# Kernel tuning notes

Measured on AMD Instinct MI355X. Metric: run time of the kernel, lower is better.

Reference implementation:

```python
import jax, jax.numpy as jnp
import numpy as np
from jax import lax

E = 16          # num_experts
CAP = 256       # capacity
MAX_IT = 3      # max_iterations
LPF = 2.0       # load_penalty_factor
DTEMP = 2.0     # diversity_temp
MIN_USAGE = 0.05
NC = 10         # num_classes
TC = 256        # trunk_channels
B = 2048
MIN_TOK = max(1, int(B * MIN_USAGE))        # 102
K_STATIC = min(B, max(CAP, MIN_TOK))        # static top-k width per expert claim


def setup_inputs() -> dict:
    key = jax.random.key(0)
    ks = jax.random.split(key, 16)
    d = {}
    d['x'] = jax.random.normal(ks[0], (B, 3, 32, 32), jnp.float32)
    chans = [(3, 32), (32, 64), (64, 128), (128, 256)]
    for i, (ci, co) in enumerate(chans, 1):
        d[f'cw{i}'] = jax.random.normal(ks[i], (co, ci, 3, 3), jnp.float32) * (1.0 / np.sqrt(ci * 9))
        d[f'cb{i}'] = jnp.zeros((co,), jnp.float32)
        d[f'g{i}'] = jnp.ones((co,), jnp.float32)
        d[f'be{i}'] = jnp.zeros((co,), jnp.float32)
        d[f'm{i}'] = jnp.zeros((co,), jnp.float32)
        d[f'v{i}'] = jnp.ones((co,), jnp.float32)
    d['gw1'] = jax.random.normal(ks[5], (E, TC, TC // 2), jnp.float32) * 0.05
    d['gb1'] = jnp.zeros((E, TC // 2), jnp.float32)
    d['gw2'] = jax.random.normal(ks[6], (E, TC // 2), jnp.float32) * 0.05
    d['gb2'] = jnp.zeros((E,), jnp.float32)
    d['cls_w'] = jax.random.normal(ks[7], (E, NC, TC), jnp.float32) * 0.01
    d['cls_b'] = jnp.zeros((E, NC), jnp.float32)
    d['usage_ema'] = jnp.ones((E,), jnp.float32) / E
    return d


def _conv_bn_relu(x, w, b, g, beta, m, v):
    y = lax.conv_general_dilated(x, w, (1, 1), 'SAME', dimension_numbers=('NCHW', 'OIHW', 'NCHW'))
    y = y + b[None, :, None, None]
    scale = (g / jnp.sqrt(v + 1e-5))[None, :, None, None]
    return jax.nn.relu((y - m[None, :, None, None]) * scale + beta[None, :, None, None])


def _maxpool2(x):
    return lax.reduce_window(x, -jnp.inf, lax.max, (1, 1, 2, 2), (1, 1, 2, 2), 'VALID')


def _forward(x, cw1, cb1, g1, be1, m1, v1, cw2, cb2, g2, be2, m2, v2,
             cw3, cb3, g3, be3, m3, v3, cw4, cb4, g4, be4, m4, v4,
             gw1, gb1, gw2, gb2, cls_w, cls_b, usage_ema):
    # trunk (eval-mode BN)
    h = _conv_bn_relu(x, cw1, cb1, g1, be1, m1, v1)
    h = _conv_bn_relu(h, cw2, cb2, g2, be2, m2, v2)
    h = _maxpool2(h)
    h = _conv_bn_relu(h, cw3, cb3, g3, be3, m3, v3)
    h = _conv_bn_relu(h, cw4, cb4, g4, be4, m4, v4)
    h = _maxpool2(h)
    feats = h.mean(axis=(2, 3))  # AdaptiveAvgPool2d(1)+Flatten -> [B, TC]

    # per-expert classifier heads
    logits_e = jnp.einsum('bd,ecd->bec', feats, cls_w) + cls_b[None]  # [B,E,NC]
    probs = jax.nn.softmax(logits_e, axis=2)
    ent = -(probs * jnp.log(jnp.clip(probs, 1e-12))).sum(axis=2)      # [B,E]
    confidence = -ent

    # per-expert gates (vectorized over experts); dropout is identity in eval
    hidden = jax.nn.relu(jnp.einsum('bd,edh->beh', feats, gw1) + gb1[None])
    expert_scores = (jnp.einsum('beh,eh->be', hidden, gw2) + gb2[None]) / DTEMP

    routing_scores = 0.6 * expert_scores + 0.4 * confidence - LPF * usage_ema[None]

    # iterative capacity-constrained routing (eval: expert order 0..E-1)
    D = jnp.zeros((B, E), bool)
    loads = jnp.zeros((E,), jnp.float32)
    avail = jnp.ones((B,), bool)
    ranks = jnp.arange(K_STATIC)
    for it in range(MAX_IT):
        # penalty from loads at the START of the iteration
        pscores = routing_scores - (it + 1) * LPF * loads[None]
        for j in range(E):
            sj = jnp.where(avail, pscores[:, j], -jnp.inf)
            vc = avail.sum().astype(jnp.int32)
            rc = jnp.maximum(0, CAP - loads[j].astype(jnp.int32))
            ntc = jnp.where((rc == 0) | (vc == 0), 0,
                            jnp.maximum(jnp.minimum(rc, vc), jnp.minimum(MIN_TOK, vc)))
            _, idx = lax.top_k(sj, K_STATIC)
            take = ranks < ntc
            claimed = jnp.zeros((B,), bool).at[idx].set(take)
            D = D.at[:, j].set(D[:, j] | claimed)
            avail = avail & ~claimed
            loads = loads.at[j].add(ntc.astype(jnp.float32))

    # fallback: sequentially assign leftover tokens to least-loaded of top-3
    def fb(carry, inp):
        Dc, lc = carry
        sc, av, i = inp
        _, t3 = lax.top_k(sc, 3)
        best = t3[jnp.argmin(lc[t3])]
        Dc = Dc.at[i, best].set(Dc[i, best] | av)
        lc = lc.at[best].add(av.astype(jnp.float32))
        return (Dc, lc), None

    (D, loads), _ = lax.scan(fb, (D, loads), (routing_scores, avail, jnp.arange(B)))

    Df = D.astype(jnp.float32)
    active = routing_scores * Df
    active = active - active.max(axis=1, keepdims=True)
    weights = jax.nn.softmax(active + (Df - 1.0) * 1e9, axis=1)
    final_logits = (weights[:, :, None] * logits_e).sum(axis=1)
    return final_logits, routing_scores, D


def reference(x, cw1, cb1, g1, be1, m1, v1, cw2, cb2, g2, be2, m2, v2,
              cw3, cb3, g3, be3, m3, v3, cw4, cb4, g4, be4, m4, v4,
              gw1, gb1, gw2, gb2, cls_w, cls_b, usage_ema):
    return _forward(x, cw1, cb1, g1, be1, m1, v1, cw2, cb2, g2, be2, m2, v2,
                    cw3, cb3, g3, be3, m3, v3, cw4, cb4, g4, be4, m4, v4,
                    gw1, gb1, gw2, gb2, cls_w, cls_b, usage_ema)
```

## Files before the change

kernel.cpp:

```cpp
#include <hip/hip_runtime.h>

typedef __attribute__((ext_vector_type(8))) short short8;
typedef __attribute__((ext_vector_type(4))) float f32x4;

__device__ __forceinline__ unsigned short f2bf(float f) {
  unsigned u = __float_as_uint(f);
  unsigned r = (u + 0x7fffu + ((u >> 16) & 1u)) >> 16;
  return (unsigned short)r;
}
__device__ __forceinline__ float bf2f(unsigned short h) {
  return __uint_as_float(((unsigned)h) << 16);
}

__global__ __launch_bounds__(256) void bnprep_kernel(
    const float* __restrict__ g, const float* __restrict__ be,
    const float* __restrict__ m, const float* __restrict__ v,
    const float* __restrict__ b, float* __restrict__ A, float* __restrict__ C, int n)
{
  int i = blockIdx.x * 256 + threadIdx.x;
  if (i < n) {
    float s = g[i] / sqrtf(v[i] + 1e-5f);
    A[i] = s;
    C[i] = (b[i] - m[i]) * s + be[i];
  }
}

__global__ __launch_bounds__(256) void wprep2_kernel(
    const float* __restrict__ w, unsigned short* __restrict__ wPk, int CO, int CI)
{
  int NCB = CI / 32, NF = CO / 16;
  int total = 9 * NCB * NF * 64;
  int idx = blockIdx.x * 256 + threadIdx.x;
  if (idx >= total) return;
  int lane = idx & 63;
  int unit = idx >> 6;
  int f = unit % NF;
  int cb = (unit / NF) % NCB;
  int s = unit / (NF * NCB);
  int co = f * 16 + (lane & 15);
  int ci0 = cb * 32 + (lane >> 4) * 8;
  long base = (long)unit * 1024 + lane * 8;
  #pragma unroll
  for (int j = 0; j < 8; ++j) {
    float v = w[((long)co * CI + ci0 + j) * 9 + s];
    unsigned short h = f2bf(v);
    unsigned short l = f2bf(v - bf2f(h));
    wPk[base + j] = h;
    wPk[base + 512 + j] = l;
  }
}

__global__ __launch_bounds__(512, 2) void conv12_kernel(
    const float* __restrict__ xin, const float* __restrict__ cw1,
    const float* __restrict__ A1p, const float* __restrict__ C1p,
    const unsigned short* __restrict__ wPk, const float* __restrict__ Ap,
    const float* __restrict__ Cp, unsigned short* __restrict__ outA)
{
  constexpr int TY = 16, TX = 32;
  constexpr int PXW = TX + 2;
  constexpr int PXT = (TY + 2) * PXW;
  constexpr int PLSTR = PXT * 8 + 8;
  constexpr int NF = 4;
  __shared__ alignas(16) unsigned short smem[8 * PLSTR];
  __shared__ alignas(16) float sx[2160];
  __shared__ alignas(16) float sw[864];

  const int nwg = gridDim.x;
  const int orig = blockIdx.x;
  const int q = nwg >> 3, r = nwg & 7;
  const int xcd = orig & 7, pos = orig >> 3;
  const int bx = (xcd < r ? xcd * (q + 1) : r * (q + 1) + (xcd - r) * q) + pos;

  const int img = bx >> 1;
  const int tY0 = (bx & 1) * 16;

  const int tid = threadIdx.x;
  const int lane = tid & 63;
  const int lx = lane & 15, kg = lane >> 4;
  const int w = tid >> 6;

  for (int i = tid; i < 2160; i += 512) {
    int c = i / 720, rem = i - c * 720;
    int yy = rem / 36, xx2 = rem - yy * 36;
    int gy = tY0 + yy - 2, gx = xx2 - 2;
    sx[i] = (gy >= 0 && gy < 32 && gx >= 0 && gx < 32)
            ? xin[(long)img * 3072 + c * 1024 + gy * 32 + gx] : 0.f;
  }
  for (int i = tid; i < 864; i += 512) {
    int co = i & 31, kk = i >> 5;
    sw[kk * 32 + co] = cw1[(long)co * 27 + kk];
  }
  __syncthreads();

  #pragma unroll 1
  for (int p = 0; p < 2; ++p) {
    int px = p * 512 + tid;
    if (px < PXT) {
      int ry = px / PXW, rx = px - ry * PXW;
      int gy = tY0 + ry - 1, gx = rx - 1;
      if (gy >= 0 && gy < 32 && gx >= 0 && gx < 32) {
        #pragma unroll 1
        for (int half = 0; half < 2; ++half) {
          float acc[16];
          #pragma unroll
          for (int j = 0; j < 16; ++j) acc[j] = 0.f;
          #pragma unroll
          for (int c = 0; c < 3; ++c) {
            #pragma unroll
            for (int k = 0; k < 9; ++k) {
              int dy = k / 3, dx = k - 3 * (k / 3);
              float iv = sx[c * 720 + (ry + dy) * 36 + rx + dx];
              const float4* w4 = (const float4*)(sw + (c * 9 + k) * 32 + half * 16);
              #pragma unroll
              for (int q2 = 0; q2 < 4; ++q2) {
                float4 wv = w4[q2];
                acc[4 * q2 + 0] += iv * wv.x; acc[4 * q2 + 1] += iv * wv.y;
                acc[4 * q2 + 2] += iv * wv.z; acc[4 * q2 + 3] += iv * wv.w;
              }
            }
          }
          #pragma unroll
          for (int j2 = 0; j2 < 2; ++j2) {
            short8 hv, lv;
            #pragma unroll
            for (int j = 0; j < 8; ++j) {
              int co = half * 16 + j2 * 8 + j;
              float vv = fmaxf(acc[j2 * 8 + j] * A1p[co] + C1p[co], 0.f);
              unsigned short h = f2bf(vv);
              hv[j] = (short)h;
              lv[j] = (short)f2bf(vv - bf2f(h));
            }
            int plane = half * 2 + j2;
            *(short8*)(smem + plane * PLSTR + px * 8) = hv;
            *(short8*)(smem + (plane + 4) * PLSTR + px * 8) = lv;
          }
        }
      } else {
        short8 zz = {0, 0, 0, 0, 0, 0, 0, 0};
        #pragma unroll
        for (int cc = 0; cc < 8; ++cc)
          *(short8*)(smem + cc * PLSTR + px * 8) = zz;
      }
    }
  }
  __syncthreads();

  f32x4 acc[4][4];
  #pragma unroll
  for (int i = 0; i < 4; ++i)
    #pragma unroll
    for (int j = 0; j < 4; ++j) acc[i][j] = (f32x4){0.f, 0.f, 0.f, 0.f};

  for (int s = 0; s < 9; ++s) {
    const int ky = s / 3, kx = s - 3 * (s / 3);
    const long ub = ((long)(s * NF)) * 1024 + lane * 8;
    short8 bh[4], bl[4];
    #pragma unroll
    for (int nf = 0; nf < 4; ++nf) {
      bh[nf] = *(const short8*)(wPk + ub + nf * 1024);
      bl[nf] = *(const short8*)(wPk + ub + nf * 1024 + 512);
    }
    #pragma unroll
    for (int mf = 0; mf < 4; ++mf) {
      const int yoff = mf >> 1;
      const int xb = (mf & 1) * 16;
      const int y = w * 2 + yoff;
      const int pxa = (y + ky) * PXW + xb + kx + lx;
      short8 ah = *(const short8*)(smem + kg * PLSTR + pxa * 8);
      short8 al = *(const short8*)(smem + (kg + 4) * PLSTR + pxa * 8);
      #pragma unroll
      for (int nf = 0; nf < 4; ++nf)
        acc[mf][nf] = __builtin_amdgcn_mfma_f32_16x16x32_bf16(ah, bh[nf], acc[mf][nf], 0, 0, 0);
      #pragma unroll
      for (int nf = 0; nf < 4; ++nf)
        acc[mf][nf] = __builtin_amdgcn_mfma_f32_16x16x32_bf16(ah, bl[nf], acc[mf][nf], 0, 0, 0);
      #pragma unroll
      for (int nf = 0; nf < 4; ++nf)
        acc[mf][nf] = __builtin_amdgcn_mfma_f32_16x16x32_bf16(al, bh[nf], acc[mf][nf], 0, 0, 0);
    }
  }
  __syncthreads();

  float Ar[4], Cr[4];
  #pragma unroll
  for (int nf = 0; nf < 4; ++nf) {
    int co = nf * 16 + lx;
    Ar[nf] = Ap[co]; Cr[nf] = Cp[co];
  }

  unsigned short* slice = smem + w * 2048;
  const int py = (tY0 >> 1) + w;
  #pragma unroll
  for (int xf = 0; xf < 2; ++xf) {
    #pragma unroll
    for (int rp = 0; rp < 2; ++rp) {
      int ox = xf * 8 + 2 * kg + rp;
      #pragma unroll
      for (int nf = 0; nf < 4; ++nf) {
        float v0 = fmaxf(fmaxf(acc[xf][nf][2 * rp], acc[xf][nf][2 * rp + 1]),
                         fmaxf(acc[xf + 2][nf][2 * rp], acc[xf + 2][nf][2 * rp + 1]));
        float vv = fmaxf(v0 * Ar[nf] + Cr[nf], 0.f);
        unsigned short h = f2bf(vv);
        unsigned short l = f2bf(vv - bf2f(h));
        slice[(ox * 2 + 0) * 64 + nf * 16 + lx] = h;
        slice[(ox * 2 + 1) * 64 + nf * 16 + lx] = l;
      }
    }
  }
  #pragma unroll
  for (int v = 0; v < 4; ++v) {
    int hoff = lane * 8 + v * 512;
    int x2 = hoff >> 7, rem = hoff & 127;
    int seg = rem >> 6, inner = rem & 63;
    short8 d = *(const short8*)(slice + hoff);
    *(short8*)(outA + ((long)img * 256 + py * 16 + x2) * 128 + seg * 64 + inner) = d;
  }
}

template<int H, int CI, int CO, int COB, int TY, int TX, int MODE>
__global__ __launch_bounds__(512, 2) void convmf4_kernel(
    const unsigned short* __restrict__ actIn, const unsigned short* __restrict__ wPk,
    const float* __restrict__ Ap, const float* __restrict__ Cp,
    void* __restrict__ outP)
{
  constexpr int NCB = CI / 32;
  constexpr int NF  = CO / 16;
  constexpr int NCOG = COB / 64;
  constexpr int NPXG = 8 / NCOG;
  constexpr int ROWS_PG = TY / NPXG;
  constexpr int FRX = TX / 16;
  constexpr int PXW = TX + 2;
  constexpr int PXT = (TY + 2) * PXW;
  constexpr int PLSTR = PXT * 8 + 8;
  constexpr int TILES_Y = H / TY;
  constexpr int CBLK = CO / COB;
  constexpr int TPI = TILES_Y * CBLK;
  constexpr int PIX_IN = 2 * CI;
  __shared__ alignas(16) unsigned short smem[8 * PLSTR];

  const int nwg = gridDim.x;
  const int orig = blockIdx.x;
  const int q = nwg >> 3, r = nwg & 7;
  const int xcd = orig & 7, pos = orig >> 3;
  const int bx = (xcd < r ? xcd * (q + 1) : r * (q + 1) + (xcd - r) * q) + pos;

  const int img = bx / TPI;
  const int sub = bx % TPI;
  const int tY0 = (sub % TILES_Y) * TY;
  const int blkco = sub / TILES_Y;

  const int tid = threadIdx.x;
  const int lane = tid & 63;
  const int lx = lane & 15, kg = lane >> 4;
  const int w = tid >> 6;
  const int pxg = w % NPXG, cog = w / NPXG;

  f32x4 acc[4][4];
  #pragma unroll
  for (int i = 0; i < 4; ++i)
    #pragma unroll
    for (int j = 0; j < 4; ++j) acc[i][j] = (f32x4){0.f, 0.f, 0.f, 0.f};

  for (int cb = 0; cb < NCB; ++cb) {
    if (cb) __syncthreads();
    for (int t2 = tid; t2 < PXT * 8; t2 += 512) {
      int px = t2 >> 3, c = t2 & 7;
      int ry = px / PXW, rx = px - ry * PXW;
      int gy = tY0 + ry - 1, gx = rx - 1;
      float4 v = (float4){0.f, 0.f, 0.f, 0.f};
      if (gy >= 0 && gy < H && gx >= 0 && gx < H) {
        int coff = (c < 4) ? (cb * 32 + c * 8) : (CI + cb * 32 + (c - 4) * 8);
        v = *(const float4*)(actIn + ((long)img * H * H + gy * H + gx) * PIX_IN + coff);
      }
      *(float4*)(smem + c * PLSTR + px * 8) = v;
    }
    __syncthreads();

    for (int s = 0; s < 9; ++s) {
      const int ky = s / 3, kx = s - 3 * (s / 3);
      const long ub = ((long)(s * NCB + cb) * NF + blkco * (COB / 16) + cog * 4) * 1024
                      + lane * 8;
      short8 bh[4], bl[4];
      #pragma unroll
      for (int nf = 0; nf < 4; ++nf) {
        bh[nf] = *(const short8*)(wPk + ub + nf * 1024);
        bl[nf] = *(const short8*)(wPk + ub + nf * 1024 + 512);
      }
      #pragma unroll
      for (int mf = 0; mf < 4; ++mf) {
        const int yoff = (FRX == 2) ? (mf >> 1) : mf;
        const int xb = (FRX == 2) ? ((mf & 1) * 16) : 0;
        const int y = pxg * ROWS_PG + yoff;
        const int pxa = (y + ky) * PXW + xb + kx + lx;
        short8 ah = *(const short8*)(smem + kg * PLSTR + pxa * 8);
        short8 al = *(const short8*)(smem + (kg + 4) * PLSTR + pxa * 8);
        #pragma unroll
        for (int nf = 0; nf < 4; ++nf)
          acc[mf][nf] = __builtin_amdgcn_mfma_f32_16x16x32_bf16(ah, bh[nf], acc[mf][nf], 0, 0, 0);
        #pragma unroll
        for (int nf = 0; nf < 4; ++nf)
          acc[mf][nf] = __builtin_amdgcn_mfma_f32_16x16x32_bf16(ah, bl[nf], acc[mf][nf], 0, 0, 0);
        #pragma unroll
        for (int nf = 0; nf < 4; ++nf)
          acc[mf][nf] = __builtin_amdgcn_mfma_f32_16x16x32_bf16(al, bh[nf], acc[mf][nf], 0, 0, 0);
      }
    }
  }
  __syncthreads();

  float Ar[4], Cr[4];
  #pragma unroll
  for (int nf = 0; nf < 4; ++nf) {
    int co = blkco * COB + cog * 64 + nf * 16 + lx;
    Ar[nf] = Ap[co]; Cr[nf] = Cp[co];
  }

  if (MODE == 0) {
    unsigned short* outA = (unsigned short*)outP;
    unsigned short* slice = smem + w * 2048;
    #pragma unroll
    for (int mf = 0; mf < 4; ++mf) {
      int y = tY0 + pxg * ROWS_PG + mf;
      #pragma unroll
      for (int rr = 0; rr < 4; ++rr) {
        int x = 4 * kg + rr;
        #pragma unroll
        for (int nf = 0; nf < 4; ++nf) {
          float vv = fmaxf(acc[mf][nf][rr] * Ar[nf] + Cr[nf], 0.f);
          unsigned short h = f2bf(vv);
          unsigned short l = f2bf(vv - bf2f(h));
          slice[(x * 2 + 0) * 64 + nf * 16 + lx] = h;
          slice[(x * 2 + 1) * 64 + nf * 16 + lx] = l;
        }
      }
      #pragma unroll
      for (int v = 0; v < 4; ++v) {
        int hoff = lane * 8 + v * 512;
        int x2 = hoff >> 7, rem = hoff & 127;
        int seg = rem >> 6, inner = rem & 63;
        short8 d = *(const short8*)(slice + hoff);
        *(short8*)(outA + ((long)img * 256 + y * 16 + x2) * (2 * CO)
                   + seg * CO + blkco * COB + cog * 64 + inner) = d;
      }
    }
  } else {
    float psum[4] = {0.f, 0.f, 0.f, 0.f};
    #pragma unroll
    for (int nf = 0; nf < 4; ++nf) {
      #pragma unroll
      for (int mfp = 0; mfp < 2; ++mfp) {
        #pragma unroll
        for (int rp = 0; rp < 2; ++rp) {
          float v = fmaxf(fmaxf(acc[2 * mfp][nf][2 * rp], acc[2 * mfp][nf][2 * rp + 1]),
                          fmaxf(acc[2 * mfp + 1][nf][2 * rp], acc[2 * mfp + 1][nf][2 * rp + 1]));
          psum[nf] += fmaxf(v * Ar[nf] + Cr[nf], 0.f);
        }
      }
    }
    #pragma unroll
    for (int nf = 0; nf < 4; ++nf) {
      psum[nf] += __shfl_xor(psum[nf], 16);
      psum[nf] += __shfl_xor(psum[nf], 32);
    }
    __syncthreads();
    float* sR = (float*)smem;
    if (kg == 0) {
      #pragma unroll
      for (int nf = 0; nf < 4; ++nf) sR[w * 64 + nf * 16 + lx] = psum[nf];
    }
    __syncthreads();
    if (tid < COB) {
      int ct = tid >> 6, ci_ = tid & 63;
      float s = 0.f;
      #pragma unroll
      for (int p = 0; p < NPXG; ++p) s += sR[(ct * NPXG + p) * 64 + ci_];
      ((float*)outP)[(long)img * 256 + blkco * COB + tid] = s * (1.f / 64.f);
    }
  }
}

__global__ __launch_bounds__(256) void heads2_kernel(
    const float* __restrict__ feats, const float* __restrict__ gw1,
    const float* __restrict__ gb1, const float* __restrict__ gw2,
    const float* __restrict__ gb2, const float* __restrict__ clsw,
    const float* __restrict__ clsb, const float* __restrict__ usage,
    float* __restrict__ logits_e, float* __restrict__ rs_out)
{
  __shared__ float sF[64 * 257];
  __shared__ float sLg[4 * 64 * 10];
  __shared__ float sRed[4 * 64];
  const int tid = threadIdx.x;
  const int b0 = blockIdx.x * 64;
  const int e  = blockIdx.y;

  for (int idx = tid; idx < 64 * 64; idx += 256) {
    int t = idx >> 6, dg = idx & 63;
    float4 v = ((const float4*)(feats + (long)(b0 + t) * 256))[dg];
    float* p = sF + t * 257 + dg * 4;
    p[0] = v.x; p[1] = v.y; p[2] = v.z; p[3] = v.w;
  }
  __syncthreads();

  const int t  = tid & 63;
  const int hw = __builtin_amdgcn_readfirstlane(tid >> 6);

  {
    float acc[10];
    #pragma unroll
    for (int c = 0; c < 10; ++c) acc[c] = 0.f;
    const float* fp = sF + t * 257 + hw * 64;
    const float* cw = clsw + (long)e * 2560 + hw * 64;
    for (int dd = 0; dd < 64; ++dd) {
      float f = fp[dd];
      #pragma unroll
      for (int c = 0; c < 10; ++c) acc[c] += f * cw[c * 256 + dd];
    }
    #pragma unroll
    for (int c = 0; c < 10; ++c) sLg[(hw * 64 + t) * 10 + c] = acc[c];
  }
  {
    float gacc[32];
    #pragma unroll
    for (int j = 0; j < 32; ++j) gacc[j] = 0.f;
    const float* wb = gw1 + ((long)e * 256) * 128 + hw * 32;
    const float* fp = sF + t * 257;
    for (int d = 0; d < 256; ++d) {
      float f = fp[d];
      const float4* w4 = (const float4*)(wb + (long)d * 128);
      #pragma unroll
      for (int qq = 0; qq < 8; ++qq) {
        float4 wv = w4[qq];
        gacc[4 * qq + 0] += f * wv.x; gacc[4 * qq + 1] += f * wv.y;
        gacc[4 * qq + 2] += f * wv.z; gacc[4 * qq + 3] += f * wv.w;
      }
    }
    float s = 0.f;
    const float* b1 = gb1 + e * 128 + hw * 32;
    const float* w2 = gw2 + e * 128 + hw * 32;
    #pragma unroll
    for (int j = 0; j < 32; ++j) s += fmaxf(gacc[j] + b1[j], 0.f) * w2[j];
    sRed[hw * 64 + t] = s;
  }
  __syncthreads();

  if (tid < 64) {
    float es = (sRed[t] + sRed[64 + t] + sRed[128 + t] + sRed[192 + t] + gb2[e]) * 0.5f;
    float lg[10];
    #pragma unroll
    for (int c = 0; c < 10; ++c)
      lg[c] = sLg[t * 10 + c] + sLg[(64 + t) * 10 + c]
            + sLg[(128 + t) * 10 + c] + sLg[(192 + t) * 10 + c] + clsb[e * 10 + c];
    float mx = lg[0];
    #pragma unroll
    for (int c = 1; c < 10; ++c) mx = fmaxf(mx, lg[c]);
    float S = 0.f, ps[10];
    #pragma unroll
    for (int c = 0; c < 10; ++c) { ps[c] = expf(lg[c] - mx); S += ps[c]; }
    float inv = 1.f / S, ent = 0.f;
    #pragma unroll
    for (int c = 0; c < 10; ++c) { float p = ps[c] * inv; ent -= p * logf(fmaxf(p, 1e-12f)); }
    float rsv = 0.6f * es + 0.4f * (-ent) - 2.0f * usage[e];
    rs_out[(long)(b0 + t) * 16 + e] = rsv;
    #pragma unroll
    for (int c = 0; c < 10; ++c)
      logits_e[((long)(b0 + t) * 16 + e) * 10 + c] = lg[c];
  }
}

__global__ __launch_bounds__(1024) void sort_kernel(
    const float* __restrict__ rs, unsigned* __restrict__ sortedIdx)
{
  __shared__ unsigned long long sk[2048];
  const int e = blockIdx.x;
  const unsigned tid = threadIdx.x;
  for (int i = tid; i < 2048; i += 1024) {
    float f = rs[(long)i * 16 + e];
    unsigned u = __float_as_uint(f);
    u ^= (u >> 31) ? 0xFFFFFFFFu : 0x80000000u;
    sk[i] = ((unsigned long long)(~u) << 32) | (unsigned)i;
  }
  for (unsigned k = 2; k <= 2048; k <<= 1) {
    for (unsigned j = k >> 1; j > 0; j >>= 1) {
      __syncthreads();
      unsigned i = ((tid & ~(j - 1)) << 1) | (tid & (j - 1));
      unsigned p = i | j;
      bool asc = ((i & k) == 0);
      unsigned long long a = sk[i], b = sk[p];
      if ((a > b) == asc) { sk[i] = b; sk[p] = a; }
    }
  }
  __syncthreads();
  for (int i = tid; i < 2048; i += 1024)
    sortedIdx[(long)e * 2048 + i] = (unsigned)(sk[i] & 0xFFFFFFFFull);
}

__global__ __launch_bounds__(64) void routing2_kernel(
    const unsigned* __restrict__ sortedIdx, const float* __restrict__ rs,
    unsigned* __restrict__ dmaskOut)
{
  __shared__ unsigned char sAvail[2048];
  __shared__ unsigned sDm[2048];
  __shared__ int sLoads[16];
  const int lane = threadIdx.x;
  for (int i = lane; i < 2048; i += 64) { sAvail[i] = 1; sDm[i] = 0; }
  if (lane < 16) sLoads[lane] = 0;
  __syncthreads();

  int vc = 2048;
  for (int it = 0; it < 3; ++it) {
    for (int j = 0; j < 16; ++j) {
      int lj = sLoads[j];
      int rc = 256 - lj; if (rc < 0) rc = 0;
      int ntc = 0;
      if (rc > 0 && vc > 0) {
        int a = rc < vc ? rc : vc;
        int b2 = vc < 102 ? vc : 102;
        ntc = a > b2 ? a : b2;
      }
      if (ntc > 0) {
        const unsigned* se = sortedIdx + (long)j * 2048;
        int taken = 0;
        for (int base = 0; base < 2048; base += 64) {
          if (taken >= ntc) break;
          unsigned tok = se[base + lane];
          int fl = sAvail[tok] ? 1 : 0;
          unsigned long long bm = __ballot(fl);
          int pre = taken + __popcll(bm & ((1ull << lane) - 1ull));
          if (fl && pre < ntc) { sAvail[tok] = 0; sDm[tok] |= (1u << j); }
          taken += (int)__popcll(bm);
          __syncthreads();
        }
        if (lane == 0) sLoads[j] = lj + ntc;
        vc -= ntc;
        __syncthreads();
      }
    }
  }

  if (vc > 0) {
    if (lane == 0) {
      for (int i = 0; i < 2048; ++i) {
        if (!sAvail[i]) continue;
        float s0 = -3.4e38f, s1 = s0, s2 = s0; int e0 = 0, e1 = 0, e2 = 0;
        for (int e = 0; e < 16; ++e) {
          float s = rs[i * 16 + e];
          if (s > s0)      { s2 = s1; e2 = e1; s1 = s0; e1 = e0; s0 = s; e0 = e; }
          else if (s > s1) { s2 = s1; e2 = e1; s1 = s;  e1 = e; }
          else if (s > s2) { s2 = s;  e2 = e; }
        }
        int best = e0, bl = sLoads[e0];
        if (sLoads[e1] < bl) { best = e1; bl = sLoads[e1]; }
        if (sLoads[e2] < bl) { best = e2; bl = sLoads[e2]; }
        sDm[i] |= (1u << best);
        sLoads[best] += 1;
      }
    }
    __syncthreads();
  }

  for (int i = lane; i < 2048; i += 64) dmaskOut[i] = sDm[i];
}

__global__ __launch_bounds__(256) void combine_kernel(
    const unsigned* __restrict__ dmask, const float* __restrict__ rs,
    const float* __restrict__ L, float* __restrict__ out, float* __restrict__ Dout)
{
  int i = blockIdx.x * 256 + threadIdx.x;
  if (i >= 2048) return;
  unsigned dm = dmask[i];
  float r[16];
  #pragma unroll
  for (int e = 0; e < 16; ++e) r[e] = rs[i * 16 + e];
  float mx = -3.4e38f;
  #pragma unroll
  for (int e = 0; e < 16; ++e) {
    float v = ((dm >> e) & 1u) ? r[e] : 0.0f;
    mx = fmaxf(mx, v);
  }
  float w[16], S = 0.f;
  #pragma unroll
  for (int e = 0; e < 16; ++e) {
    w[e] = ((dm >> e) & 1u) ? expf(r[e] - mx) : 0.0f;
    S += w[e];
  }
  float inv = 1.f / S;
  #pragma unroll
  for (int c = 0; c < 10; ++c) {
    float a = 0.f;
    #pragma unroll
    for (int e = 0; e < 16; ++e) a += w[e] * L[((long)i * 16 + e) * 10 + c];
    out[i * 10 + c] = a * inv;
  }
  #pragma unroll
  for (int e = 0; e < 16; ++e)
    Dout[(long)i * 16 + e] = ((dm >> e) & 1u) ? 1.0f : 0.0f;
}

extern "C" void kernel_launch(void* const* d_in, const int* in_sizes, int n_in,
                              void* d_out, int out_size, void* d_ws, size_t ws_size,
                              hipStream_t stream)
{
  const float* x    = (const float*)d_in[0];
  const float* cw1  = (const float*)d_in[1];
  const float* cb1  = (const float*)d_in[2];
  const float* g1   = (const float*)d_in[3];
  const float* be1  = (const float*)d_in[4];
  const float* m1   = (const float*)d_in[5];
  const float* v1   = (const float*)d_in[6];
  const float* cw2  = (const float*)d_in[7];
  const float* cb2  = (const float*)d_in[8];
  const float* g2   = (const float*)d_in[9];
  const float* be2  = (const float*)d_in[10];
  const float* m2   = (const float*)d_in[11];
  const float* v2   = (const float*)d_in[12];
  const float* cw3  = (const float*)d_in[13];
  const float* cb3  = (const float*)d_in[14];
  const float* g3   = (const float*)d_in[15];
  const float* be3  = (const float*)d_in[16];
  const float* m3   = (const float*)d_in[17];
  const float* v3   = (const float*)d_in[18];
  const float* cw4  = (const float*)d_in[19];
  const float* cb4  = (const float*)d_in[20];
  const float* g4   = (const float*)d_in[21];
  const float* be4  = (const float*)d_in[22];
  const float* m4   = (const float*)d_in[23];
  const float* v4   = (const float*)d_in[24];
  const float* gw1  = (const float*)d_in[25];
  const float* gb1  = (const float*)d_in[26];
  const float* gw2  = (const float*)d_in[27];
  const float* gb2  = (const float*)d_in[28];
  const float* clsw = (const float*)d_in[29];
  const float* clsb = (const float*)d_in[30];
  const float* usage = (const float*)d_in[31];

  float* out = (float*)d_out;
  float* ws  = (float*)d_ws;

  float* A1 = ws + 0;   float* C1 = ws + 32;
  float* A2 = ws + 64;  float* C2 = ws + 128;
  float* A3 = ws + 192; float* C3 = ws + 320;
  float* A4 = ws + 448; float* C4 = ws + 704;
  float* feats   = ws + 1024;
  float* logitsE = ws + 525312;
  unsigned* sortedIdx = (unsigned*)(ws + 852992);
  unsigned* dmask     = (unsigned*)(ws + 885760);
  unsigned short* wPk2 = (unsigned short*)(ws + 887808);
  unsigned short* wPk3 = (unsigned short*)(ws + 906240);
  unsigned short* wPk4 = (unsigned short*)(ws + 979968);
  const long bufBase = 1274880;

  long wsFloats = (long)(ws_size / 4);
  long availF = wsFloats - bufBase;
  long chunkL = availF / 49152;
  int chunk = (int)(chunkL < 1 ? 1 : (chunkL > 2048 ? 2048 : chunkL));

  bnprep_kernel<<<1, 256, 0, stream>>>(g1, be1, m1, v1, cb1, A1, C1, 32);
  bnprep_kernel<<<1, 256, 0, stream>>>(g2, be2, m2, v2, cb2, A2, C2, 64);
  bnprep_kernel<<<1, 256, 0, stream>>>(g3, be3, m3, v3, cb3, A3, C3, 128);
  bnprep_kernel<<<1, 256, 0, stream>>>(g4, be4, m4, v4, cb4, A4, C4, 256);
  wprep2_kernel<<<(2304 + 255) / 256, 256, 0, stream>>>(cw2, wPk2, 64, 32);
  wprep2_kernel<<<(9216 + 255) / 256, 256, 0, stream>>>(cw3, wPk3, 128, 64);
  wprep2_kernel<<<(36864 + 255) / 256, 256, 0, stream>>>(cw4, wPk4, 256, 128);

  unsigned short* bufA = (unsigned short*)(ws + bufBase);
  unsigned short* bufB = bufA + (long)chunk * 65536;

  for (int ib = 0; ib < 2048; ib += chunk) {
    int n = 2048 - ib; if (n > chunk) n = chunk;
    conv12_kernel<<<dim3(n * 2), 512, 0, stream>>>(
        x + (long)ib * 3072, cw1, A1, C1, wPk2, A2, C2, bufB);
    convmf4_kernel<16, 64, 128, 128, 16, 16, 0>
        <<<dim3(n), 512, 0, stream>>>(bufB, wPk3, A3, C3, bufA);
    convmf4_kernel<16, 128, 256, 128, 16, 16, 2>
        <<<dim3(n * 2), 512, 0, stream>>>(bufA, wPk4, A4, C4, feats + (long)ib * 256);
  }

  float* rsOut = out + 20480;
  heads2_kernel<<<dim3(32, 16), 256, 0, stream>>>(feats, gw1, gb1, gw2, gb2,
                                                  clsw, clsb, usage, logitsE, rsOut);
  sort_kernel<<<16, 1024, 0, stream>>>(rsOut, sortedIdx);
  routing2_kernel<<<1, 64, 0, stream>>>(sortedIdx, rsOut, dmask);
  combine_kernel<<<8, 256, 0, stream>>>(dmask, rsOut, logitsE, out, out + 53248);
}
```

Measured before the change: 1.420 ms.

## Add dedicated conv4 kernel covering all output channels per image with XCD-aware remap

Replaces the generic conv4 launch (two workgroups per image, each covering half the output channels) with a specialized kernel where one 512-thread workgroup computes all 256 output channels for an image. Each wave holds a 4x8 tile of MFMA accumulators, so every staged activation tile in shared memory is reused across all output channels rather than being loaded twice. It also remaps block indices so consecutive images land on the same XCD, which should improve L2 locality. The costs are higher register pressure (128 accumulator registers, launch_bounds 512,1), fewer workgroups in the grid, and weights read directly from global memory.

```diff
diff --git a/kernel.cpp b/kernel.cpp
--- a/kernel.cpp
+++ b/kernel.cpp
@@ -379,6 +379,143 @@
   }
 }
 
+__global__ __launch_bounds__(512, 1) void convmf5_kernel(
+    const unsigned short* __restrict__ actIn, const unsigned short* __restrict__ wPk,
+    const float* __restrict__ Ap, const float* __restrict__ Cp,
+    float* __restrict__ feats)
+{
+  constexpr int CI = 128, CO = 256, H = 16;
+  constexpr int NCB = 4, NF = 16;
+  constexpr int PXW = 18, PXT = 324;
+  constexpr int PLSTR = PXT * 8 + 8;
+  constexpr int PIX_IN = 2 * CI;
+  __shared__ alignas(16) unsigned short smem[8 * PLSTR];
+
+  const int nwg = gridDim.x;
+  const int orig = blockIdx.x;
+  const int q = nwg >> 3, r = nwg & 7;
+  const int xcd = orig & 7, pos = orig >> 3;
+  const int img = (xcd < r ? xcd * (q + 1) : r * (q + 1) + (xcd - r) * q) + pos;
+
+  const int tid = threadIdx.x;
+  const int lane = tid & 63;
+  const int lx = lane & 15, kg = lane >> 4;
+  const int w = tid >> 6;
+  const int pxg = w >> 1;
+  const int cog = w & 1;
+
+  f32x4 acc[4][8];
+  #pragma unroll
+  for (int i = 0; i < 4; ++i)
+    #pragma unroll
+    for (int j = 0; j < 8; ++j) acc[i][j] = (f32x4){0.f, 0.f, 0.f, 0.f};
+
+  for (int cb = 0; cb < NCB; ++cb) {
+    if (cb) __syncthreads();
+    for (int t2 = tid; t2 < PXT * 8; t2 += 512) {
+      int px = t2 >> 3, c = t2 & 7;
+      int ry = px / PXW, rx = px - ry * PXW;
+      int gy = ry - 1, gx = rx - 1;
+      float4 v = (float4){0.f, 0.f, 0.f, 0.f};
+      if (gy >= 0 && gy < H && gx >= 0 && gx < H) {
+        int coff = (c < 4) ? (cb * 32 + c * 8) : (CI + cb * 32 + (c - 4) * 8);
+        v = *(const float4*)(actIn + ((long)img * H * H + gy * H + gx) * PIX_IN + coff);
+      }
+      *(float4*)(smem + c * PLSTR + px * 8) = v;
+    }
+    __syncthreads();
+
+    for (int s = 0; s < 9; ++s) {
+      const int ky = s / 3, kx = s - 3 * (s / 3);
+      short8 ah[4], al[4];
+      #pragma unroll
+      for (int mf = 0; mf < 4; ++mf) {
+        const int pxa = (pxg * 4 + mf + ky) * PXW + kx + lx;
+        ah[mf] = *(const short8*)(smem + kg * PLSTR + pxa * 8);
+        al[mf] = *(const short8*)(smem + (kg + 4) * PLSTR + pxa * 8);
+      }
+      const long ub = ((long)(s * NCB + cb) * NF + cog * 8) * 1024 + lane * 8;
+      {
+        short8 bh[4], bl[4];
+        #pragma unroll
+        for (int nf = 0; nf < 4; ++nf) {
+          bh[nf] = *(const short8*)(wPk + ub + nf * 1024);
+          bl[nf] = *(const short8*)(wPk + ub + nf * 1024 + 512);
+        }
+        #pragma unroll
+        for (int mf = 0; mf < 4; ++mf) {
+          #pragma unroll
+          for (int nf = 0; nf < 4; ++nf)
+            acc[mf][nf] = __builtin_amdgcn_mfma_f32_16x16x32_bf16(ah[mf], bh[nf], acc[mf][nf], 0, 0, 0);
+          #pragma unroll
+          for (int nf = 0; nf < 4; ++nf)
+            acc[mf][nf] = __builtin_amdgcn_mfma_f32_16x16x32_bf16(ah[mf], bl[nf], acc[mf][nf], 0, 0, 0);
+          #pragma unroll
+          for (int nf = 0; nf < 4; ++nf)
+            acc[mf][nf] = __builtin_amdgcn_mfma_f32_16x16x32_bf16(al[mf], bh[nf], acc[mf][nf], 0, 0, 0);
+        }
+      }
+      {
+        short8 bh[4], bl[4];
+        #pragma unroll
+        for (int nf = 0; nf < 4; ++nf) {
+          bh[nf] = *(const short8*)(wPk + ub + (4 + nf) * 1024);
+          bl[nf] = *(const short8*)(wPk + ub + (4 + nf) * 1024 + 512);
+        }
+        #pragma unroll
+        for (int mf = 0; mf < 4; ++mf) {
+          #pragma unroll
+          for (int nf = 0; nf < 4; ++nf)
+            acc[mf][4 + nf] = __builtin_amdgcn_mfma_f32_16x16x32_bf16(ah[mf], bh[nf], acc[mf][4 + nf], 0, 0, 0);
+          #pragma unroll
+          for (int nf = 0; nf < 4; ++nf)
+            acc[mf][4 + nf] = __builtin_amdgcn_mfma_f32_16x16x32_bf16(ah[mf], bl[nf], acc[mf][4 + nf], 0, 0, 0);
+          #pragma unroll
+          for (int nf = 0; nf < 4; ++nf)
+            acc[mf][4 + nf] = __builtin_amdgcn_mfma_f32_16x16x32_bf16(al[mf], bh[nf], acc[mf][4 + nf], 0, 0, 0);
+        }
+      }
+    }
+  }
+  __syncthreads();
+
+  float psum[8];
+  #pragma unroll
+  for (int j = 0; j < 8; ++j) psum[j] = 0.f;
+  #pragma unroll
+  for (int j = 0; j < 8; ++j) {
+    int co = (cog * 8 + j) * 16 + lx;
+    float Ar = Ap[co], Cr = Cp[co];
+    #pragma unroll
+    for (int u = 0; u < 2; ++u) {
+      #pragma unroll
+      for (int v = 0; v < 2; ++v) {
+        float vm = fmaxf(fmaxf(acc[2 * u][j][2 * v], acc[2 * u][j][2 * v + 1]),
+                         fmaxf(acc[2 * u + 1][j][2 * v], acc[2 * u + 1][j][2 * v + 1]));
+        psum[j] += fmaxf(vm * Ar + Cr, 0.f);
+      }
+    }
+  }
+  #pragma unroll
+  for (int j = 0; j < 8; ++j) {
+    psum[j] += __shfl_xor(psum[j], 16);
+    psum[j] += __shfl_xor(psum[j], 32);
+  }
+  float* sR = (float*)smem;
+  if (kg == 0) {
+    #pragma unroll
+    for (int j = 0; j < 8; ++j) sR[w * 128 + j * 16 + lx] = psum[j];
+  }
+  __syncthreads();
+  if (tid < 256) {
+    int cogT = tid >> 7, cl = tid & 127;
+    float s = 0.f;
+    #pragma unroll
+    for (int p = 0; p < 4; ++p) s += sR[(p * 2 + cogT) * 128 + cl];
+    feats[(long)img * 256 + tid] = s * (1.f / 64.f);
+  }
+}
+
 __global__ __launch_bounds__(256) void heads2_kernel(
     const float* __restrict__ feats, const float* __restrict__ gw1,
     const float* __restrict__ gb1, const float* __restrict__ gw2,
@@ -671,8 +808,8 @@
         x + (long)ib * 3072, cw1, A1, C1, wPk2, A2, C2, bufB);
     convmf4_kernel<16, 64, 128, 128, 16, 16, 0>
         <<<dim3(n), 512, 0, stream>>>(bufB, wPk3, A3, C3, bufA);
-    convmf4_kernel<16, 128, 256, 128, 16, 16, 2>
-        <<<dim3(n * 2), 512, 0, stream>>>(bufA, wPk4, A4, C4, feats + (long)ib * 256);
+    convmf5_kernel<<<dim3(n), 512, 0, stream>>>(bufA, wPk4, A4, C4,
+                                                feats + (long)ib * 256);
   }
 
   float* rsOut = out + 20480;
```

Result: no change. 1.404 ms (-1.2%).
